# Kernel optimization log

Measured on AMD Instinct MI355X. Metric: run time of the kernel, lower is better.

## Reference

```python
import jax, jax.numpy as jnp
import numpy as np

D_MODEL = 1024
NUM_HEADS = 16
HEAD_DIM = D_MODEL // NUM_HEADS
D_FF = 4 * D_MODEL


def _linear_params(key, d_in, d_out):
    kw, kb = jax.random.split(key)
    bound = 1.0 / np.sqrt(d_in)
    W = jax.random.uniform(kw, (d_in, d_out), minval=-bound, maxval=bound, dtype=jnp.float32)
    b = jax.random.uniform(kb, (d_out,), minval=-bound, maxval=bound, dtype=jnp.float32)
    return W, b


def setup_inputs() -> dict:
    key = jax.random.key(0)
    ks = jax.random.split(key, 6)
    x = jax.random.normal(ks[0], (4, 2048, D_MODEL), dtype=jnp.float32)
    qkv_w, qkv_b = _linear_params(ks[1], D_MODEL, 3 * D_MODEL)
    out_w, out_b = _linear_params(ks[2], D_MODEL, D_MODEL)
    ffn1_w, ffn1_b = _linear_params(ks[3], D_MODEL, D_FF)
    ffn2_w, ffn2_b = _linear_params(ks[4], D_FF, D_MODEL)
    ln1_g = jnp.ones((D_MODEL,), jnp.float32); ln1_b = jnp.zeros((D_MODEL,), jnp.float32)
    ln2_g = jnp.ones((D_MODEL,), jnp.float32); ln2_b = jnp.zeros((D_MODEL,), jnp.float32)
    return {
        "x": x,
        "qkv_w": qkv_w, "qkv_b": qkv_b,
        "out_w": out_w, "out_b": out_b,
        "ffn1_w": ffn1_w, "ffn1_b": ffn1_b,
        "ffn2_w": ffn2_w, "ffn2_b": ffn2_b,
        "ln1_g": ln1_g, "ln1_b": ln1_b,
        "ln2_g": ln2_g, "ln2_b": ln2_b,
    }


def _layer_norm(x, g, b, eps=1e-5):
    mu = jnp.mean(x, axis=-1, keepdims=True)
    var = jnp.mean(jnp.square(x - mu), axis=-1, keepdims=True)
    return (x - mu) * jax.lax.rsqrt(var + eps) * g + b


def reference(x, qkv_w, qkv_b, out_w, out_b, ffn1_w, ffn1_b, ffn2_w, ffn2_b,
              ln1_g, ln1_b, ln2_g, ln2_b):
    B, S, D = x.shape
    H, Hd = NUM_HEADS, HEAD_DIM
    normed = _layer_norm(x, ln1_g, ln1_b)
    qkv = normed @ qkv_w + qkv_b                      # [B,S,3D]
    qkv = qkv.reshape(B, S, 3, H, Hd)
    q = jnp.transpose(qkv[:, :, 0], (0, 2, 1, 3))     # [B,H,S,Hd]
    k = jnp.transpose(qkv[:, :, 1], (0, 2, 1, 3))
    v = jnp.transpose(qkv[:, :, 2], (0, 2, 1, 3))
    scores = jnp.einsum('bhqd,bhkd->bhqk', q, k) / np.sqrt(Hd).astype(np.float32)
    causal = jnp.tril(jnp.ones((S, S), dtype=bool))
    scores = jnp.where(causal[None, None], scores, -jnp.inf)
    attn = jax.nn.softmax(scores, axis=-1)
    attn_out = jnp.einsum('bhqk,bhkd->bhqd', attn, v)  # [B,H,S,Hd]
    attn_out = jnp.transpose(attn_out, (0, 2, 1, 3)).reshape(B, S, D)
    attn_out = attn_out @ out_w + out_b
    x = x + attn_out
    h = _layer_norm(x, ln2_g, ln2_b)
    h = jax.nn.gelu(h @ ffn1_w + ffn1_b, approximate=False)
    h = h @ ffn2_w + ffn2_b
    return x + h
```

## Files before the change

### kernel.cpp

```cpp
#include <hip/hip_runtime.h>
#include <hip/hip_bf16.h>
#include <math.h>

typedef __attribute__((ext_vector_type(8))) short short8;
typedef __attribute__((ext_vector_type(4))) float f32x4;

__device__ __forceinline__ float bf2f(unsigned short u) {
    union { unsigned int i; float f; } c; c.i = ((unsigned int)u) << 16; return c.f;
}
__device__ __forceinline__ unsigned short f2bf(float f) {
    union { float f; unsigned int i; } c; c.f = f;
    unsigned int i = c.i;
    unsigned int r = (i + 0x7FFFu + ((i >> 16) & 1u)) >> 16;
    return (unsigned short)r;
}
__device__ __forceinline__ float ldf(const float* p, size_t i) { return p[i]; }
__device__ __forceinline__ float ldf(const unsigned short* p, size_t i) { return bf2f(p[i]); }
__device__ __forceinline__ void stf(float* p, size_t i, float v) { p[i] = v; }
__device__ __forceinline__ void stf(unsigned short* p, size_t i, float v) { p[i] = f2bf(v); }

__device__ __forceinline__ void glds16(const unsigned short* g, unsigned short* l) {
    __builtin_amdgcn_global_load_lds(
        (const __attribute__((address_space(1))) unsigned int*)g,
        (__attribute__((address_space(3))) unsigned int*)l, 16, 0, 0);
}

__global__ __launch_bounds__(256) void ln_f32_kernel(
    const float* __restrict__ x, const float* __restrict__ g,
    const float* __restrict__ b, unsigned short* __restrict__ out) {
    const int row = blockIdx.x;
    const int t = threadIdx.x;
    const float* xr = x + (size_t)row * 1024;
    float4 raw = ((const float4*)xr)[t];
    float v0 = raw.x, v1 = raw.y, v2 = raw.z, v3 = raw.w;
    float s = v0 + v1 + v2 + v3;
    float ss = v0 * v0 + v1 * v1 + v2 * v2 + v3 * v3;
    for (int off = 32; off > 0; off >>= 1) {
        s += __shfl_down(s, off);
        ss += __shfl_down(ss, off);
    }
    __shared__ float red[8];
    __shared__ float stat[2];
    const int wave = t >> 6, lane = t & 63;
    if (lane == 0) { red[wave] = s; red[4 + wave] = ss; }
    __syncthreads();
    if (t == 0) {
        float st = red[0] + red[1] + red[2] + red[3];
        float sst = red[4] + red[5] + red[6] + red[7];
        float mu = st * (1.0f / 1024.0f);
        float var = sst * (1.0f / 1024.0f) - mu * mu;
        stat[0] = mu; stat[1] = rsqrtf(var + 1e-5f);
    }
    __syncthreads();
    const float mu = stat[0], rstd = stat[1];
    float4 gr = ((const float4*)g)[t];
    float4 br = ((const float4*)b)[t];
    ushort4 o;
    o.x = f2bf((v0 - mu) * rstd * gr.x + br.x);
    o.y = f2bf((v1 - mu) * rstd * gr.y + br.y);
    o.z = f2bf((v2 - mu) * rstd * gr.z + br.z);
    o.w = f2bf((v3 - mu) * rstd * gr.w + br.w);
    ((ushort4*)(out + (size_t)row * 1024))[t] = o;
}

__global__ __launch_bounds__(256) void ln_bf16_kernel(
    const unsigned short* __restrict__ x, const float* __restrict__ g,
    const float* __restrict__ b, unsigned short* __restrict__ out) {
    const int row = blockIdx.x;
    const int t = threadIdx.x;
    const unsigned short* xr = x + (size_t)row * 1024;
    ushort4 raw = ((const ushort4*)xr)[t];
    float v0 = bf2f(raw.x), v1 = bf2f(raw.y), v2 = bf2f(raw.z), v3 = bf2f(raw.w);
    float s = v0 + v1 + v2 + v3;
    float ss = v0 * v0 + v1 * v1 + v2 * v2 + v3 * v3;
    for (int off = 32; off > 0; off >>= 1) {
        s += __shfl_down(s, off);
        ss += __shfl_down(ss, off);
    }
    __shared__ float red[8];
    __shared__ float stat[2];
    const int wave = t >> 6, lane = t & 63;
    if (lane == 0) { red[wave] = s; red[4 + wave] = ss; }
    __syncthreads();
    if (t == 0) {
        float st = red[0] + red[1] + red[2] + red[3];
        float sst = red[4] + red[5] + red[6] + red[7];
        float mu = st * (1.0f / 1024.0f);
        float var = sst * (1.0f / 1024.0f) - mu * mu;
        stat[0] = mu; stat[1] = rsqrtf(var + 1e-5f);
    }
    __syncthreads();
    const float mu = stat[0], rstd = stat[1];
    float4 gr = ((const float4*)g)[t];
    float4 br = ((const float4*)b)[t];
    ushort4 o;
    o.x = f2bf((v0 - mu) * rstd * gr.x + br.x);
    o.y = f2bf((v1 - mu) * rstd * gr.y + br.y);
    o.z = f2bf((v2 - mu) * rstd * gr.z + br.z);
    o.w = f2bf((v3 - mu) * rstd * gr.w + br.w);
    ((ushort4*)(out + (size_t)row * 1024))[t] = o;
}

__global__ __launch_bounds__(256) void transpose_cast_kernel(
    const float* __restrict__ in, unsigned short* __restrict__ out, int R, int C) {
    __shared__ unsigned short tile[32][33];
    const int bx = blockIdx.x * 32, by = blockIdx.y * 32;
    const int tx = threadIdx.x & 31, ty = threadIdx.x >> 5;
    for (int i = 0; i < 32; i += 8)
        tile[ty + i][tx] = f2bf(in[(size_t)(by + ty + i) * C + bx + tx]);
    __syncthreads();
    for (int i = 0; i < 32; i += 8)
        out[(size_t)(bx + ty + i) * R + by + tx] = tile[tx][ty + i];
}

enum { EPI_QKV = 0, EPI_RES = 1, EPI_GELU = 2 };

template <int EPI, typename RT, typename OT>
__global__ __launch_bounds__(256) void gemm_bt(
    const unsigned short* __restrict__ A, const unsigned short* __restrict__ Bt,
    const float* __restrict__ bias, const RT* __restrict__ res,
    OT* __restrict__ o0, unsigned short* __restrict__ o1,
    unsigned short* __restrict__ o2, int M, int N, int K) {
    __shared__ __align__(16) unsigned short As[128 * 32];
    __shared__ __align__(16) unsigned short Bs[128 * 32];
    const int t = threadIdx.x;
    const int wave = t >> 6, lane = t & 63;
    const int lr = lane & 15, lq = lane >> 4;
    const int wm = (wave >> 1) * 64, wn = (wave & 1) * 64;
    const int m0 = blockIdx.y * 128, n0 = blockIdx.x * 128;
    f32x4 acc[4][4] = {};
    const int arow = t >> 2, acol = (t & 3) << 3;
    const unsigned short* ag = A + (size_t)(m0 + arow) * K + acol;
    const unsigned short* bg = Bt + (size_t)(n0 + arow) * K + acol;
    const size_t rstride = (size_t)64 * K;
    for (int k0 = 0; k0 < K; k0 += 32) {
        glds16(ag + k0, As + t * 8);
        glds16(ag + rstride + k0, As + 2048 + t * 8);
        glds16(bg + k0, Bs + t * 8);
        glds16(bg + rstride + k0, Bs + 2048 + t * 8);
        __syncthreads();
        short8 af[4], bfr[4];
#pragma unroll
        for (int i = 0; i < 4; i++) af[i] = *(const short8*)(As + (wm + i * 16 + lr) * 32 + lq * 8);
#pragma unroll
        for (int i = 0; i < 4; i++) bfr[i] = *(const short8*)(Bs + (wn + i * 16 + lr) * 32 + lq * 8);
#pragma unroll
        for (int mi = 0; mi < 4; mi++)
#pragma unroll
            for (int ni = 0; ni < 4; ni++)
                acc[mi][ni] = __builtin_amdgcn_mfma_f32_16x16x32_bf16(af[mi], bfr[ni], acc[mi][ni], 0, 0, 0);
        __syncthreads();
    }
#pragma unroll
    for (int ni = 0; ni < 4; ni++) {
        const int col = n0 + wn + ni * 16 + lr;
        const float bv = bias[col];
#pragma unroll
        for (int mi = 0; mi < 4; mi++) {
#pragma unroll
            for (int r = 0; r < 4; r++) {
                const int row = m0 + wm + mi * 16 + lq * 4 + r;
                float val = acc[mi][ni][r] + bv;
                if (EPI == EPI_QKV) {
                    const int which = col >> 10, rem = col & 1023;
                    const int hn = rem >> 6, d = rem & 63;
                    const int bb = row >> 11, s = row & 2047;
                    const size_t bh = (size_t)(bb * 16 + hn);
                    if (which == 0) stf((unsigned short*)o0, (bh * 2048 + s) * 64 + d, val);
                    else if (which == 1) o1[(bh * 2048 + s) * 64 + d] = f2bf(val);
                    else o2[(bh * 64 + d) * 2048 + s] = f2bf(val);
                } else if (EPI == EPI_RES) {
                    val += ldf(res, (size_t)row * N + col);
                    stf(o0, (size_t)row * N + col, val);
                } else {
                    val = 0.5f * val * (1.0f + erff(val * 0.70710678118654752f));
                    stf(o0, (size_t)row * N + col, val);
                }
            }
        }
    }
}

__global__ __launch_bounds__(256) void attn_kernel(
    const unsigned short* __restrict__ qb, const unsigned short* __restrict__ kb,
    const unsigned short* __restrict__ vtb, unsigned short* __restrict__ aout) {
    const int bx = blockIdx.x;
    const int qblk = (bx & 1) ? (15 - (bx >> 1)) : (bx >> 1);
    const int bh = blockIdx.y;
    const int bidx = bh >> 4, h = bh & 15;
    const int t = threadIdx.x, wave = t >> 6, lane = t & 63;
    const int lr = lane & 15, lq = lane >> 4;
    __shared__ __align__(16) unsigned short Ks[64 * 68];
    __shared__ __align__(16) unsigned short Vs[64 * 68];
    __shared__ __align__(16) unsigned short Ps[4][32 * 68];

    const unsigned short* qbase = qb + ((size_t)bh * 2048 + qblk * 128 + wave * 32) * 64;
    short8 qf[2][2];
#pragma unroll
    for (int f = 0; f < 2; f++)
#pragma unroll
        for (int c = 0; c < 2; c++)
            qf[f][c] = *(const short8*)(qbase + (f * 16 + lr) * 64 + c * 32 + lq * 8);

    f32x4 acc[2][4] = {};
    float m_i[2][4], l_i[2][4];
#pragma unroll
    for (int f = 0; f < 2; f++)
#pragma unroll
        for (int r = 0; r < 4; r++) { m_i[f][r] = -1e30f; l_i[f][r] = 0.0f; }

    const unsigned short* kbase = kb + (size_t)bh * 2048 * 64;
    const unsigned short* vbase = vtb + (size_t)bh * 64 * 2048;
    const int srow = t >> 3, scol = (t & 7) * 8;
    const int wave_qmax = qblk * 128 + wave * 32 + 31;
    const int nkt = 2 * (qblk + 1);
    for (int kt = 0; kt < nkt; kt++) {
        const unsigned short* kg = kbase + kt * 4096;
        short8 kr0 = *(const short8*)(kg + t * 8);
        short8 kr1 = *(const short8*)(kg + 2048 + t * 8);
        short8 vr0 = *(const short8*)(vbase + (size_t)srow * 2048 + kt * 64 + scol);
        short8 vr1 = *(const short8*)(vbase + (size_t)(32 + srow) * 2048 + kt * 64 + scol);
        __syncthreads();
        *(short8*)(Ks + srow * 68 + scol) = kr0;
        *(short8*)(Ks + (32 + srow) * 68 + scol) = kr1;
        *(short8*)(Vs + srow * 68 + scol) = vr0;
        *(short8*)(Vs + (32 + srow) * 68 + scol) = vr1;
        __syncthreads();
        if (kt * 64 <= wave_qmax) {
            f32x4 sa[2][4];
#pragma unroll
            for (int ni = 0; ni < 4; ni++) {
                short8 kf0 = *(const short8*)(Ks + (ni * 16 + lr) * 68 + lq * 8);
                short8 kf1 = *(const short8*)(Ks + (ni * 16 + lr) * 68 + 32 + lq * 8);
#pragma unroll
                for (int f = 0; f < 2; f++) {
                    f32x4 z = {};
                    z = __builtin_amdgcn_mfma_f32_16x16x32_bf16(qf[f][0], kf0, z, 0, 0, 0);
                    sa[f][ni] = __builtin_amdgcn_mfma_f32_16x16x32_bf16(qf[f][1], kf1, z, 0, 0, 0);
                }
            }
#pragma unroll
            for (int f = 0; f < 2; f++) {
                const int qrow0 = qblk * 128 + wave * 32 + f * 16 + lq * 4;
                float mcur[4] = {-1e30f, -1e30f, -1e30f, -1e30f};
#pragma unroll
                for (int ni = 0; ni < 4; ni++) {
                    const int kcol = kt * 64 + ni * 16 + lr;
#pragma unroll
                    for (int r = 0; r < 4; r++) {
                        float sv = sa[f][ni][r] * 0.125f;
                        if (kcol > qrow0 + r) sv = -1e30f;
                        sa[f][ni][r] = sv;
                        mcur[r] = fmaxf(mcur[r], sv);
                    }
                }
                float alpha[4], rsum[4];
#pragma unroll
                for (int r = 0; r < 4; r++) {
#pragma unroll
                    for (int off = 1; off < 16; off <<= 1) mcur[r] = fmaxf(mcur[r], __shfl_xor(mcur[r], off));
                    const float mn = fmaxf(m_i[f][r], mcur[r]);
                    alpha[r] = __expf(m_i[f][r] - mn);
                    m_i[f][r] = mn;
                    rsum[r] = 0.0f;
                }
#pragma unroll
                for (int ni = 0; ni < 4; ni++)
#pragma unroll
                    for (int r = 0; r < 4; r++) {
                        const float p = __expf(sa[f][ni][r] - m_i[f][r]);
                        Ps[wave][(f * 16 + lq * 4 + r) * 68 + ni * 16 + lr] = f2bf(p);
                        rsum[r] += p;
                    }
#pragma unroll
                for (int r = 0; r < 4; r++) {
#pragma unroll
                    for (int off = 1; off < 16; off <<= 1) rsum[r] += __shfl_xor(rsum[r], off);
                    l_i[f][r] = l_i[f][r] * alpha[r] + rsum[r];
#pragma unroll
                    for (int ni = 0; ni < 4; ni++) acc[f][ni][r] *= alpha[r];
                }
            }
            short8 pf[2][2];
#pragma unroll
            for (int f = 0; f < 2; f++)
#pragma unroll
                for (int c = 0; c < 2; c++)
                    pf[f][c] = *(const short8*)(&Ps[wave][(f * 16 + lr) * 68 + c * 32 + lq * 8]);
#pragma unroll
            for (int ni = 0; ni < 4; ni++) {
                short8 vf0 = *(const short8*)(Vs + (ni * 16 + lr) * 68 + lq * 8);
                short8 vf1 = *(const short8*)(Vs + (ni * 16 + lr) * 68 + 32 + lq * 8);
#pragma unroll
                for (int f = 0; f < 2; f++) {
                    acc[f][ni] = __builtin_amdgcn_mfma_f32_16x16x32_bf16(pf[f][0], vf0, acc[f][ni], 0, 0, 0);
                    acc[f][ni] = __builtin_amdgcn_mfma_f32_16x16x32_bf16(pf[f][1], vf1, acc[f][ni], 0, 0, 0);
                }
            }
        }
    }
#pragma unroll
    for (int f = 0; f < 2; f++)
#pragma unroll
        for (int ni = 0; ni < 4; ni++)
#pragma unroll
            for (int r = 0; r < 4; r++) {
                const int q = qblk * 128 + wave * 32 + f * 16 + lq * 4 + r;
                const size_t token = (size_t)bidx * 2048 + q;
                aout[token * 1024 + h * 64 + ni * 16 + lr] = f2bf(acc[f][ni][r] / l_i[f][r]);
            }
}

extern "C" void kernel_launch(void* const* d_in, const int* in_sizes, int n_in,
                              void* d_out, int out_size, void* d_ws, size_t ws_size,
                              hipStream_t stream) {
    const float* x      = (const float*)d_in[0];
    const float* qkv_w  = (const float*)d_in[1];
    const float* qkv_b  = (const float*)d_in[2];
    const float* out_w  = (const float*)d_in[3];
    const float* out_b  = (const float*)d_in[4];
    const float* ffn1_w = (const float*)d_in[5];
    const float* ffn1_b = (const float*)d_in[6];
    const float* ffn2_w = (const float*)d_in[7];
    const float* ffn2_b = (const float*)d_in[8];
    const float* ln1_g  = (const float*)d_in[9];
    const float* ln1_b  = (const float*)d_in[10];
    const float* ln2_g  = (const float*)d_in[11];
    const float* ln2_b  = (const float*)d_in[12];
    float* out = (float*)d_out;
    char* W = (char*)d_ws;

    unsigned short* normed = (unsigned short*)(W);
    unsigned short* x1     = (unsigned short*)(W + 16777216);
    unsigned short* qbuf   = (unsigned short*)(W + 33554432);
    unsigned short* kbuf   = (unsigned short*)(W + 50331648);
    unsigned short* vbuf   = (unsigned short*)(W + 67108864);
    unsigned short* attnb  = (unsigned short*)(W + 83886080);
    unsigned short* hff    = (unsigned short*)(W + 33554432);
    unsigned short* qkv_wt = (unsigned short*)(W + 100663296);
    unsigned short* out_wt = (unsigned short*)(W + 106954752);
    unsigned short* f1_wt  = (unsigned short*)(W + 109051904);
    unsigned short* f2_wt  = (unsigned short*)(W + 117440512);

    transpose_cast_kernel<<<dim3(3072 / 32, 1024 / 32), 256, 0, stream>>>(qkv_w, qkv_wt, 1024, 3072);
    transpose_cast_kernel<<<dim3(1024 / 32, 1024 / 32), 256, 0, stream>>>(out_w, out_wt, 1024, 1024);
    transpose_cast_kernel<<<dim3(4096 / 32, 1024 / 32), 256, 0, stream>>>(ffn1_w, f1_wt, 1024, 4096);
    transpose_cast_kernel<<<dim3(1024 / 32, 4096 / 32), 256, 0, stream>>>(ffn2_w, f2_wt, 4096, 1024);

    ln_f32_kernel<<<dim3(8192), 256, 0, stream>>>(x, ln1_g, ln1_b, normed);
    gemm_bt<EPI_QKV, float, unsigned short><<<dim3(3072 / 128, 8192 / 128), 256, 0, stream>>>(
        normed, qkv_wt, qkv_b, nullptr, qbuf, kbuf, vbuf, 8192, 3072, 1024);
    attn_kernel<<<dim3(16, 64), 256, 0, stream>>>(qbuf, kbuf, vbuf, attnb);
    gemm_bt<EPI_RES, float, unsigned short><<<dim3(1024 / 128, 8192 / 128), 256, 0, stream>>>(
        attnb, out_wt, out_b, x, x1, nullptr, nullptr, 8192, 1024, 1024);
    ln_bf16_kernel<<<dim3(8192), 256, 0, stream>>>(x1, ln2_g, ln2_b, normed);
    gemm_bt<EPI_GELU, float, unsigned short><<<dim3(4096 / 128, 8192 / 128), 256, 0, stream>>>(
        normed, f1_wt, ffn1_b, nullptr, hff, nullptr, nullptr, 8192, 4096, 1024);
    gemm_bt<EPI_RES, unsigned short, float><<<dim3(1024 / 128, 8192 / 128), 256, 0, stream>>>(
        hff, f2_wt, ffn2_b, x1, out, nullptr, nullptr, 8192, 1024, 4096);
}
```

Measured before the change: 730.4 us.

## Pair causal q-blocks per attention block, prefetch K/V, narrow N-tile for skinny GEMMs

Result: faster. 692.9 us (-5.1%).

```diff
diff --git a/kernel.cpp b/kernel.cpp
--- a/kernel.cpp
+++ b/kernel.cpp
@@ -18,6 +18,7 @@
 __device__ __forceinline__ float ldf(const unsigned short* p, size_t i) { return bf2f(p[i]); }
 __device__ __forceinline__ void stf(float* p, size_t i, float v) { p[i] = v; }
 __device__ __forceinline__ void stf(unsigned short* p, size_t i, float v) { p[i] = f2bf(v); }
+__device__ __forceinline__ float fexp2(float x) { return __builtin_amdgcn_exp2f(x); }
 
 __device__ __forceinline__ void glds16(const unsigned short* g, unsigned short* l) {
     __builtin_amdgcn_global_load_lds(
@@ -115,20 +116,21 @@
 
 enum { EPI_QKV = 0, EPI_RES = 1, EPI_GELU = 2 };
 
-template <int EPI, typename RT, typename OT>
+template <int EPI, int BN, typename RT, typename OT>
 __global__ __launch_bounds__(256) void gemm_bt(
     const unsigned short* __restrict__ A, const unsigned short* __restrict__ Bt,
     const float* __restrict__ bias, const RT* __restrict__ res,
     OT* __restrict__ o0, unsigned short* __restrict__ o1,
     unsigned short* __restrict__ o2, int M, int N, int K) {
     __shared__ __align__(16) unsigned short As[128 * 32];
-    __shared__ __align__(16) unsigned short Bs[128 * 32];
+    __shared__ __align__(16) unsigned short Bs[BN * 32];
+    constexpr int NF = BN / 32;
     const int t = threadIdx.x;
     const int wave = t >> 6, lane = t & 63;
     const int lr = lane & 15, lq = lane >> 4;
-    const int wm = (wave >> 1) * 64, wn = (wave & 1) * 64;
-    const int m0 = blockIdx.y * 128, n0 = blockIdx.x * 128;
-    f32x4 acc[4][4] = {};
+    const int wm = (wave >> 1) * 64, wn = (wave & 1) * (BN / 2);
+    const int m0 = blockIdx.y * 128, n0 = blockIdx.x * BN;
+    f32x4 acc[4][NF] = {};
     const int arow = t >> 2, acol = (t & 3) << 3;
     const unsigned short* ag = A + (size_t)(m0 + arow) * K + acol;
     const unsigned short* bg = Bt + (size_t)(n0 + arow) * K + acol;
@@ -137,22 +139,22 @@
         glds16(ag + k0, As + t * 8);
         glds16(ag + rstride + k0, As + 2048 + t * 8);
         glds16(bg + k0, Bs + t * 8);
-        glds16(bg + rstride + k0, Bs + 2048 + t * 8);
+        if (BN == 128) glds16(bg + rstride + k0, Bs + 2048 + t * 8);
         __syncthreads();
-        short8 af[4], bfr[4];
+        short8 af[4], bfr[NF];
 #pragma unroll
         for (int i = 0; i < 4; i++) af[i] = *(const short8*)(As + (wm + i * 16 + lr) * 32 + lq * 8);
 #pragma unroll
-        for (int i = 0; i < 4; i++) bfr[i] = *(const short8*)(Bs + (wn + i * 16 + lr) * 32 + lq * 8);
+        for (int i = 0; i < NF; i++) bfr[i] = *(const short8*)(Bs + (wn + i * 16 + lr) * 32 + lq * 8);
 #pragma unroll
         for (int mi = 0; mi < 4; mi++)
 #pragma unroll
-            for (int ni = 0; ni < 4; ni++)
+            for (int ni = 0; ni < NF; ni++)
                 acc[mi][ni] = __builtin_amdgcn_mfma_f32_16x16x32_bf16(af[mi], bfr[ni], acc[mi][ni], 0, 0, 0);
         __syncthreads();
     }
 #pragma unroll
-    for (int ni = 0; ni < 4; ni++) {
+    for (int ni = 0; ni < NF; ni++) {
         const int col = n0 + wn + ni * 16 + lr;
         const float bv = bias[col];
 #pragma unroll
@@ -185,7 +187,6 @@
     const unsigned short* __restrict__ qb, const unsigned short* __restrict__ kb,
     const unsigned short* __restrict__ vtb, unsigned short* __restrict__ aout) {
     const int bx = blockIdx.x;
-    const int qblk = (bx & 1) ? (15 - (bx >> 1)) : (bx >> 1);
     const int bh = blockIdx.y;
     const int bidx = bh >> 4, h = bh & 15;
     const int t = threadIdx.x, wave = t >> 6, lane = t & 63;
@@ -193,122 +194,141 @@
     __shared__ __align__(16) unsigned short Ks[64 * 68];
     __shared__ __align__(16) unsigned short Vs[64 * 68];
     __shared__ __align__(16) unsigned short Ps[4][32 * 68];
-
-    const unsigned short* qbase = qb + ((size_t)bh * 2048 + qblk * 128 + wave * 32) * 64;
-    short8 qf[2][2];
-#pragma unroll
-    for (int f = 0; f < 2; f++)
-#pragma unroll
-        for (int c = 0; c < 2; c++)
-            qf[f][c] = *(const short8*)(qbase + (f * 16 + lr) * 64 + c * 32 + lq * 8);
-
-    f32x4 acc[2][4] = {};
-    float m_i[2][4], l_i[2][4];
-#pragma unroll
-    for (int f = 0; f < 2; f++)
-#pragma unroll
-        for (int r = 0; r < 4; r++) { m_i[f][r] = -1e30f; l_i[f][r] = 0.0f; }
-
     const unsigned short* kbase = kb + (size_t)bh * 2048 * 64;
     const unsigned short* vbase = vtb + (size_t)bh * 64 * 2048;
     const int srow = t >> 3, scol = (t & 7) * 8;
-    const int wave_qmax = qblk * 128 + wave * 32 + 31;
-    const int nkt = 2 * (qblk + 1);
-    for (int kt = 0; kt < nkt; kt++) {
-        const unsigned short* kg = kbase + kt * 4096;
-        short8 kr0 = *(const short8*)(kg + t * 8);
-        short8 kr1 = *(const short8*)(kg + 2048 + t * 8);
-        short8 vr0 = *(const short8*)(vbase + (size_t)srow * 2048 + kt * 64 + scol);
-        short8 vr1 = *(const short8*)(vbase + (size_t)(32 + srow) * 2048 + kt * 64 + scol);
-        __syncthreads();
-        *(short8*)(Ks + srow * 68 + scol) = kr0;
-        *(short8*)(Ks + (32 + srow) * 68 + scol) = kr1;
-        *(short8*)(Vs + srow * 68 + scol) = vr0;
-        *(short8*)(Vs + (32 + srow) * 68 + scol) = vr1;
-        __syncthreads();
-        if (kt * 64 <= wave_qmax) {
-            f32x4 sa[2][4];
-#pragma unroll
-            for (int ni = 0; ni < 4; ni++) {
-                short8 kf0 = *(const short8*)(Ks + (ni * 16 + lr) * 68 + lq * 8);
-                short8 kf1 = *(const short8*)(Ks + (ni * 16 + lr) * 68 + 32 + lq * 8);
+    const float kQScale = 0.125f * 1.44269504088896f;
+
+    for (int phase = 0; phase < 2; phase++) {
+        const int qblk = phase ? (15 - bx) : bx;
+        const unsigned short* qbase = qb + ((size_t)bh * 2048 + qblk * 128 + wave * 32) * 64;
+        short8 qf[2][2];
+#pragma unroll
+        for (int f = 0; f < 2; f++)
+#pragma unroll
+            for (int c = 0; c < 2; c++) {
+                short8 raw = *(const short8*)(qbase + (f * 16 + lr) * 64 + c * 32 + lq * 8);
+                short8 sc;
+#pragma unroll
+                for (int j = 0; j < 8; j++)
+                    sc[j] = (short)f2bf(bf2f((unsigned short)raw[j]) * kQScale);
+                qf[f][c] = sc;
+            }
+        f32x4 acc[2][4] = {};
+        float m_i[2][4], l_i[2][4];
+#pragma unroll
+        for (int f = 0; f < 2; f++)
+#pragma unroll
+            for (int r = 0; r < 4; r++) { m_i[f][r] = -1e30f; l_i[f][r] = 0.0f; }
+        const int wave_q0 = qblk * 128 + wave * 32;
+        const int nkt = 2 * (qblk + 1);
+        short8 kr0 = *(const short8*)(kbase + t * 8);
+        short8 kr1 = *(const short8*)(kbase + 2048 + t * 8);
+        short8 vr0 = *(const short8*)(vbase + (size_t)srow * 2048 + scol);
+        short8 vr1 = *(const short8*)(vbase + (size_t)(32 + srow) * 2048 + scol);
+        for (int kt = 0; kt < nkt; kt++) {
+            __syncthreads();
+            *(short8*)(Ks + srow * 68 + scol) = kr0;
+            *(short8*)(Ks + (32 + srow) * 68 + scol) = kr1;
+            *(short8*)(Vs + srow * 68 + scol) = vr0;
+            *(short8*)(Vs + (32 + srow) * 68 + scol) = vr1;
+            __syncthreads();
+            if (kt + 1 < nkt) {
+                const unsigned short* kg = kbase + (kt + 1) * 4096;
+                kr0 = *(const short8*)(kg + t * 8);
+                kr1 = *(const short8*)(kg + 2048 + t * 8);
+                vr0 = *(const short8*)(vbase + (size_t)srow * 2048 + (kt + 1) * 64 + scol);
+                vr1 = *(const short8*)(vbase + (size_t)(32 + srow) * 2048 + (kt + 1) * 64 + scol);
+            }
+            if (kt * 64 <= wave_q0 + 31) {
+                f32x4 sa[2][4];
+#pragma unroll
+                for (int ni = 0; ni < 4; ni++) {
+                    short8 kf0 = *(const short8*)(Ks + (ni * 16 + lr) * 68 + lq * 8);
+                    short8 kf1 = *(const short8*)(Ks + (ni * 16 + lr) * 68 + 32 + lq * 8);
+#pragma unroll
+                    for (int f = 0; f < 2; f++) {
+                        f32x4 z = {};
+                        z = __builtin_amdgcn_mfma_f32_16x16x32_bf16(qf[f][0], kf0, z, 0, 0, 0);
+                        sa[f][ni] = __builtin_amdgcn_mfma_f32_16x16x32_bf16(qf[f][1], kf1, z, 0, 0, 0);
+                    }
+                }
+                const bool needmask = (kt * 64 + 63 > wave_q0);
+                if (needmask) {
+#pragma unroll
+                    for (int f = 0; f < 2; f++) {
+                        const int qrow0 = wave_q0 + f * 16 + lq * 4;
+#pragma unroll
+                        for (int ni = 0; ni < 4; ni++) {
+                            const int kcol = kt * 64 + ni * 16 + lr;
+#pragma unroll
+                            for (int r = 0; r < 4; r++)
+                                if (kcol > qrow0 + r) sa[f][ni][r] = -1e30f;
+                        }
+                    }
+                }
 #pragma unroll
                 for (int f = 0; f < 2; f++) {
-                    f32x4 z = {};
-                    z = __builtin_amdgcn_mfma_f32_16x16x32_bf16(qf[f][0], kf0, z, 0, 0, 0);
-                    sa[f][ni] = __builtin_amdgcn_mfma_f32_16x16x32_bf16(qf[f][1], kf1, z, 0, 0, 0);
-                }
-            }
-#pragma unroll
-            for (int f = 0; f < 2; f++) {
-                const int qrow0 = qblk * 128 + wave * 32 + f * 16 + lq * 4;
-                float mcur[4] = {-1e30f, -1e30f, -1e30f, -1e30f};
+                    float mcur[4], alpha[4], rsum[4];
+#pragma unroll
+                    for (int r = 0; r < 4; r++)
+                        mcur[r] = fmaxf(fmaxf(sa[f][0][r], sa[f][1][r]), fmaxf(sa[f][2][r], sa[f][3][r]));
+#pragma unroll
+                    for (int r = 0; r < 4; r++) {
+#pragma unroll
+                        for (int off = 1; off < 16; off <<= 1) mcur[r] = fmaxf(mcur[r], __shfl_xor(mcur[r], off));
+                        const float mn = fmaxf(m_i[f][r], mcur[r]);
+                        alpha[r] = fexp2(m_i[f][r] - mn);
+                        m_i[f][r] = mn;
+                        rsum[r] = 0.0f;
+                    }
+#pragma unroll
+                    for (int ni = 0; ni < 4; ni++)
+#pragma unroll
+                        for (int r = 0; r < 4; r++) {
+                            const float p = fexp2(sa[f][ni][r] - m_i[f][r]);
+                            Ps[wave][(f * 16 + lq * 4 + r) * 68 + ni * 16 + lr] = f2bf(p);
+                            rsum[r] += p;
+                        }
+#pragma unroll
+                    for (int r = 0; r < 4; r++) {
+#pragma unroll
+                        for (int off = 1; off < 16; off <<= 1) rsum[r] += __shfl_xor(rsum[r], off);
+                        l_i[f][r] = l_i[f][r] * alpha[r] + rsum[r];
+#pragma unroll
+                        for (int ni = 0; ni < 4; ni++) acc[f][ni][r] *= alpha[r];
+                    }
+                }
+                short8 pf[2][2];
+#pragma unroll
+                for (int f = 0; f < 2; f++)
+#pragma unroll
+                    for (int c = 0; c < 2; c++)
+                        pf[f][c] = *(const short8*)(&Ps[wave][(f * 16 + lr) * 68 + c * 32 + lq * 8]);
 #pragma unroll
                 for (int ni = 0; ni < 4; ni++) {
-                    const int kcol = kt * 64 + ni * 16 + lr;
-#pragma unroll
-                    for (int r = 0; r < 4; r++) {
-                        float sv = sa[f][ni][r] * 0.125f;
-                        if (kcol > qrow0 + r) sv = -1e30f;
-                        sa[f][ni][r] = sv;
-                        mcur[r] = fmaxf(mcur[r], sv);
-                    }
-                }
-                float alpha[4], rsum[4];
-#pragma unroll
-                for (int r = 0; r < 4; r++) {
-#pragma unroll
-                    for (int off = 1; off < 16; off <<= 1) mcur[r] = fmaxf(mcur[r], __shfl_xor(mcur[r], off));
-                    const float mn = fmaxf(m_i[f][r], mcur[r]);
-                    alpha[r] = __expf(m_i[f][r] - mn);
-                    m_i[f][r] = mn;
-                    rsum[r] = 0.0f;
-                }
-#pragma unroll
-                for (int ni = 0; ni < 4; ni++)
-#pragma unroll
-                    for (int r = 0; r < 4; r++) {
-                        const float p = __expf(sa[f][ni][r] - m_i[f][r]);
-                        Ps[wave][(f * 16 + lq * 4 + r) * 68 + ni * 16 + lr] = f2bf(p);
-                        rsum[r] += p;
-                    }
-#pragma unroll
-                for (int r = 0; r < 4; r++) {
-#pragma unroll
-                    for (int off = 1; off < 16; off <<= 1) rsum[r] += __shfl_xor(rsum[r], off);
-                    l_i[f][r] = l_i[f][r] * alpha[r] + rsum[r];
-#pragma unroll
-                    for (int ni = 0; ni < 4; ni++) acc[f][ni][r] *= alpha[r];
-                }
-            }
-            short8 pf[2][2];
-#pragma unroll
-            for (int f = 0; f < 2; f++)
-#pragma unroll
-                for (int c = 0; c < 2; c++)
-                    pf[f][c] = *(const short8*)(&Ps[wave][(f * 16 + lr) * 68 + c * 32 + lq * 8]);
-#pragma unroll
-            for (int ni = 0; ni < 4; ni++) {
-                short8 vf0 = *(const short8*)(Vs + (ni * 16 + lr) * 68 + lq * 8);
-                short8 vf1 = *(const short8*)(Vs + (ni * 16 + lr) * 68 + 32 + lq * 8);
-#pragma unroll
-                for (int f = 0; f < 2; f++) {
-                    acc[f][ni] = __builtin_amdgcn_mfma_f32_16x16x32_bf16(pf[f][0], vf0, acc[f][ni], 0, 0, 0);
-                    acc[f][ni] = __builtin_amdgcn_mfma_f32_16x16x32_bf16(pf[f][1], vf1, acc[f][ni], 0, 0, 0);
+                    short8 vf0 = *(const short8*)(Vs + (ni * 16 + lr) * 68 + lq * 8);
+                    short8 vf1 = *(const short8*)(Vs + (ni * 16 + lr) * 68 + 32 + lq * 8);
+#pragma unroll
+                    for (int f = 0; f < 2; f++) {
+                        acc[f][ni] = __builtin_amdgcn_mfma_f32_16x16x32_bf16(pf[f][0], vf0, acc[f][ni], 0, 0, 0);
+                        acc[f][ni] = __builtin_amdgcn_mfma_f32_16x16x32_bf16(pf[f][1], vf1, acc[f][ni], 0, 0, 0);
+                    }
                 }
             }
         }
-    }
-#pragma unroll
-    for (int f = 0; f < 2; f++)
-#pragma unroll
-        for (int ni = 0; ni < 4; ni++)
+#pragma unroll
+        for (int f = 0; f < 2; f++)
 #pragma unroll
             for (int r = 0; r < 4; r++) {
+                const float rinv = 1.0f / l_i[f][r];
                 const int q = qblk * 128 + wave * 32 + f * 16 + lq * 4 + r;
                 const size_t token = (size_t)bidx * 2048 + q;
-                aout[token * 1024 + h * 64 + ni * 16 + lr] = f2bf(acc[f][ni][r] / l_i[f][r]);
-            }
+#pragma unroll
+                for (int ni = 0; ni < 4; ni++)
+                    aout[token * 1024 + h * 64 + ni * 16 + lr] = f2bf(acc[f][ni][r] * rinv);
+            }
+    }
 }
 
 extern "C" void kernel_launch(void* const* d_in, const int* in_sizes, int n_in,
@@ -348,14 +368,14 @@
     transpose_cast_kernel<<<dim3(1024 / 32, 4096 / 32), 256, 0, stream>>>(ffn2_w, f2_wt, 4096, 1024);
 
     ln_f32_kernel<<<dim3(8192), 256, 0, stream>>>(x, ln1_g, ln1_b, normed);
-    gemm_bt<EPI_QKV, float, unsigned short><<<dim3(3072 / 128, 8192 / 128), 256, 0, stream>>>(
+    gemm_bt<EPI_QKV, 128, float, unsigned short><<<dim3(3072 / 128, 8192 / 128), 256, 0, stream>>>(
         normed, qkv_wt, qkv_b, nullptr, qbuf, kbuf, vbuf, 8192, 3072, 1024);
-    attn_kernel<<<dim3(16, 64), 256, 0, stream>>>(qbuf, kbuf, vbuf, attnb);
-    gemm_bt<EPI_RES, float, unsigned short><<<dim3(1024 / 128, 8192 / 128), 256, 0, stream>>>(
+    attn_kernel<<<dim3(8, 64), 256, 0, stream>>>(qbuf, kbuf, vbuf, attnb);
+    gemm_bt<EPI_RES, 64, float, unsigned short><<<dim3(1024 / 64, 8192 / 128), 256, 0, stream>>>(
         attnb, out_wt, out_b, x, x1, nullptr, nullptr, 8192, 1024, 1024);
     ln_bf16_kernel<<<dim3(8192), 256, 0, stream>>>(x1, ln2_g, ln2_b, normed);
-    gemm_bt<EPI_GELU, float, unsigned short><<<dim3(4096 / 128, 8192 / 128), 256, 0, stream>>>(
+    gemm_bt<EPI_GELU, 128, float, unsigned short><<<dim3(4096 / 128, 8192 / 128), 256, 0, stream>>>(
         normed, f1_wt, ffn1_b, nullptr, hff, nullptr, nullptr, 8192, 4096, 1024);
-    gemm_bt<EPI_RES, unsigned short, float><<<dim3(1024 / 128, 8192 / 128), 256, 0, stream>>>(
+    gemm_bt<EPI_RES, 64, unsigned short, float><<<dim3(1024 / 64, 8192 / 128), 256, 0, stream>>>(
         hff, f2_wt, ffn2_b, x1, out, nullptr, nullptr, 8192, 1024, 4096);
 }
```
